# Performance work log

Measured on AMD Instinct MI355X. Metric: run time of the kernel, lower is better.

## Reference

```python
import jax, jax.numpy as jnp
import numpy as np

B, LENC, LDEC, DIN, H = 256, 48, 10, 512, 512
LOOK = 10  # hard-coded look_back in the torch module
START = LDEC + LENC - LOOK  # initial label index


def setup_inputs() -> dict:
    key = jax.random.key(0)
    ks = jax.random.split(key, 28)
    s = 0.05
    n = lambda k, shape: jax.random.normal(k, shape, jnp.float32) * s
    return {
        "input_p_q": jax.random.normal(ks[0], (B, LENC, DIN), jnp.float32),
        "label_p": jax.random.normal(ks[1], (B, LENC + LDEC), jnp.float32),
        # LSTMCell_spatial_encoder (input DIN)
        "Wih_sp": n(ks[2], (4 * H, DIN)), "Whh_sp": n(ks[3], (4 * H, H)),
        "bih_sp": n(ks[4], (4 * H,)), "bhh_sp": n(ks[5], (4 * H,)),
        # LSTMcell_target_encoder (input 1+H)
        "Wih_tg": n(ks[6], (4 * H, 1 + H)), "Whh_tg": n(ks[7], (4 * H, H)),
        "bih_tg": n(ks[8], (4 * H,)), "bhh_tg": n(ks[9], (4 * H,)),
        # LSTM_mid (single layer, input H)
        "Wih_mid": n(ks[10], (4 * H, H)), "Whh_mid": n(ks[11], (4 * H, H)),
        "bih_mid": n(ks[12], (4 * H,)), "bhh_mid": n(ks[13], (4 * H,)),
        # spatial attention
        "Wi_w": n(ks[14], (H, DIN)), "Wi_b": n(ks[15], (H,)),
        "We_w": n(ks[16], (H, 2 * H)), "Wt_w": n(ks[17], (H, 2 * H)),
        "Vd_w": n(ks[18], (DIN, H)), "Vd_b": n(ks[19], (DIN,)),
        # temporal attention
        "Wx_w": n(ks[20], (H, H)), "Wx_b": n(ks[21], (H,)),
        "Wh_w": n(ks[22], (H, 2 * H)),
        "V_w": n(ks[23], (1, H)), "V_b": n(ks[24], (1,)),
        "reg_w": n(ks[25], (1, H)), "reg_b": n(ks[26], (1,)),
    }


def _lstm_cell(x, h, c, Wih, Whh, b):
    # torch LSTMCell: gates ordered (i, f, g, o)
    g = x @ Wih.T + h @ Whh.T + b
    i, f, gg, o = jnp.split(g, 4, axis=1)
    c2 = jax.nn.sigmoid(f) * c + jax.nn.sigmoid(i) * jnp.tanh(gg)
    return jax.nn.sigmoid(o) * jnp.tanh(c2), c2


def reference(input_p_q, label_p, Wih_sp, Whh_sp, bih_sp, bhh_sp,
              Wih_tg, Whh_tg, bih_tg, bhh_tg, Wih_mid, Whh_mid, bih_mid, bhh_mid,
              Wi_w, Wi_b, We_w, Wt_w, Vd_w, Vd_b, Wx_w, Wx_b, Wh_w, V_w, V_b,
              reg_w, reg_b):
    Bsz = input_p_q.shape[0]
    b_sp = bih_sp + bhh_sp
    b_tg = bih_tg + bhh_tg
    b_mid = bih_mid + bhh_mid
    # Precompute spatial_attention_Wi(inputs) for all encoder steps: [LENC, B, H]
    wi_seq = jnp.transpose(jnp.einsum('bld,hd->blh', input_p_q, Wi_w) + Wi_b, (1, 0, 2))
    x_seq = jnp.transpose(input_p_q, (1, 0, 2))  # [LENC, B, DIN]
    zeros = jnp.zeros((Bsz, H), input_p_q.dtype)

    def outer_step(carry, _):
        ht, ct, dec_in, lab = carry
        x = jnp.concatenate([lab[:, None], dec_in], axis=1)          # [B, 1+H]
        ht, ct = _lstm_cell(x, ht, ct, Wih_tg, Whh_tg, b_tg)
        target = ht @ reg_w.T + reg_b                                # [B, 1]
        lab = target[:, 0]
        wt = jnp.concatenate([ht, ct], axis=1) @ Wt_w.T              # [B, H], fixed per inner loop

        def sp_step(c2, xs):
            he, ce = c2
            wi_x, x_i = xs
            score = jnp.tanh(jnp.concatenate([he, ce], axis=1) @ We_w.T + wi_x + wt) @ Vd_w.T + Vd_b
            x_mod = x_i * jax.nn.softmax(score, axis=1)              # [B, DIN]
            he, ce = _lstm_cell(x_mod, he, ce, Wih_sp, Whh_sp, b_sp)
            return (he, ce), he

        _, mid = jax.lax.scan(sp_step, (zeros, zeros), (wi_seq, x_seq))  # [LENC, B, H]

        def mid_step(c2, x_i):
            h, c = c2
            h, c = _lstm_cell(x_i, h, c, Wih_mid, Whh_mid, b_mid)
            return (h, c), h

        _, mid2 = jax.lax.scan(mid_step, (zeros, zeros), mid)        # [LENC, B, H]
        mid2 = jnp.transpose(mid2, (1, 0, 2))                        # [B, LENC, H]
        wh = jnp.concatenate([ht, ct], axis=1) @ Wh_w.T              # [B, H]
        sc = jnp.tanh(wh[:, None, :] + mid2 @ Wx_w.T + Wx_b) @ V_w.T + V_b  # [B, LENC, 1]
        # NOTE: torch uses the RAW (un-softmaxed) scores for the bmm
        dec_in = jnp.einsum('bl,blh->bh', sc[..., 0], mid2)          # [B, H]
        return (ht, ct, dec_in, lab), target[:, 0]

    init = (zeros, zeros, zeros, label_p[:, START])
    _, targets = jax.lax.scan(outer_step, init, None, length=LOOK)   # [LOOK, B]
    return targets.T                                                 # [B, LDEC]
```

## Files before the change

### kernel.cpp

```cpp
#include <hip/hip_runtime.h>
#include <math.h>

#define Bsz   256
#define Hd    512
#define Din   512
#define Lenc  48
#define Look  10
#define G4    2048
#define LabStride 58
#define StartIdx  48

typedef unsigned short u16;
using bfrag = __attribute__((ext_vector_type(8))) short;
using f32x4 = __attribute__((ext_vector_type(4))) float;

#define MFMA16(a,b,c) __builtin_amdgcn_mfma_f32_16x16x32_bf16((a),(b),(c),0,0,0)

__device__ __forceinline__ u16 f2bf(float f){
  unsigned u = __float_as_uint(f);
  u += 0x7FFFu + ((u>>16)&1u);
  return (u16)(u>>16);
}
__device__ __forceinline__ float bf2f(u16 h){ return __uint_as_float(((unsigned)h)<<16); }
__device__ __forceinline__ float sigm(float x){ return 1.f/(1.f+__expf(-x)); }

template<int K>
__device__ __forceinline__ void mm32(const u16* __restrict__ A, int lda,
                                     const u16* __restrict__ W, int ldw,
                                     f32x4* acc, int lane){
  const int rr = lane & 15, ko = (lane>>4)<<3;
  const u16* a0 = A + (size_t)rr*lda + ko;
  const u16* a1 = a0 + 16*(size_t)lda;
  const u16* w0 = W + (size_t)rr*ldw + ko;
  const u16* w1 = w0 + 16*(size_t)ldw;
#pragma unroll
  for(int k=0;k<K;k+=32){
    bfrag av0 = *(const bfrag*)(a0+k);
    bfrag av1 = *(const bfrag*)(a1+k);
    bfrag wv0 = *(const bfrag*)(w0+k);
    bfrag wv1 = *(const bfrag*)(w1+k);
    acc[0] = MFMA16(av0,wv0,acc[0]);
    acc[1] = MFMA16(av0,wv1,acc[1]);
    acc[2] = MFMA16(av1,wv0,acc[2]);
    acc[3] = MFMA16(av1,wv1,acc[3]);
  }
}

__global__ void k_cvt(const float* __restrict__ s, u16* __restrict__ d, int n){
  for(int i=blockIdx.x*blockDim.x+threadIdx.x; i<n; i+=gridDim.x*blockDim.x) d[i]=f2bf(s[i]);
}

__global__ void k_cvt_tg(const float* __restrict__ s, u16* __restrict__ d, float* __restrict__ c0){
  int stride=gridDim.x*blockDim.x;
  for(int i=blockIdx.x*blockDim.x+threadIdx.x; i<G4*Hd; i+=stride){
    int n=i>>9, k=i&511;
    d[i]=f2bf(s[n*513+1+k]);
  }
  for(int n=blockIdx.x*blockDim.x+threadIdx.x; n<G4; n+=stride) c0[n]=s[n*513];
}

__global__ void k_init(const float* __restrict__ label, float* __restrict__ lab){
  int b=threadIdx.x;
  if(b<Bsz) lab[b]=label[b*LabStride+StartIdx];
}

__global__ __launch_bounds__(64) void k_wi(const u16* __restrict__ inpb, const u16* __restrict__ Wi,
                     const float* __restrict__ Wib, float* __restrict__ wi_seq){
  int lane=threadIdx.x;
  int r0=blockIdx.x*32, h0=blockIdx.y*32;
  f32x4 acc[4]={};
  mm32<Din>(inpb+(size_t)r0*Din, Din, Wi+(size_t)h0*Din, Din, acc, lane);
  int cr=(lane>>4)*4, cc=lane&15;
  for(int mi=0;mi<2;mi++)for(int ni=0;ni<2;ni++){
    int h=h0+ni*16+cc; float bias=Wib[h];
    f32x4 a=acc[mi*2+ni];
    for(int j=0;j<4;j++){
      int g=r0+mi*16+cr+j;
      int b=g/Lenc, l=g-b*Lenc;
      wi_seq[((size_t)l*Bsz+b)*Hd + h] = a[j]+bias;
    }
  }
}


__global__ __launch_bounds__(128) void k_spre(const u16* __restrict__ he, const u16* __restrict__ ce,
      const u16* __restrict__ We, const float* __restrict__ wi_l, const float* __restrict__ wt,
      u16* __restrict__ spre, int zhc){
  int lane=threadIdx.x&63, wid=threadIdx.x>>6;
  int b0=blockIdx.x*32, h0=blockIdx.y*32;
  f32x4 acc[4]={};
  if(!zhc){
    if(wid==0) mm32<Hd>(he+(size_t)b0*Hd, Hd, We+(size_t)h0*1024,     1024, acc, lane);
    else       mm32<Hd>(ce+(size_t)b0*Hd, Hd, We+(size_t)h0*1024+512, 1024, acc, lane);
  }
  __shared__ f32x4 red[4*64];
  if(wid==1){ for(int i=0;i<4;i++) red[i*64+lane]=acc[i]; }
  __syncthreads();
  if(wid!=0) return;
  for(int i=0;i<4;i++) acc[i]+=red[i*64+lane];
  int cr=(lane>>4)*4, cc=lane&15;
  for(int mi=0;mi<2;mi++)for(int ni=0;ni<2;ni++){
    int h=h0+ni*16+cc;
    f32x4 a=acc[mi*2+ni];
    for(int j=0;j<4;j++){
      int b=b0+mi*16+cr+j;
      size_t ix=(size_t)b*Hd+h;
      spre[ix]=f2bf(tanhf(a[j]+wi_l[ix]+wt[ix]));
    }
  }
}

__global__ __launch_bounds__(128) void k_dual(const u16* __restrict__ A1, const u16* __restrict__ A2,
      const u16* __restrict__ W, float* __restrict__ C){
  int lane=threadIdx.x&63, wid=threadIdx.x>>6;
  int b0=blockIdx.x*32, h0=blockIdx.y*32;
  f32x4 acc[4]={};
  if(wid==0) mm32<Hd>(A1+(size_t)b0*Hd, Hd, W+(size_t)h0*1024,     1024, acc, lane);
  else       mm32<Hd>(A2+(size_t)b0*Hd, Hd, W+(size_t)h0*1024+512, 1024, acc, lane);
  __shared__ f32x4 red[4*64];
  if(wid==1){ for(int i=0;i<4;i++) red[i*64+lane]=acc[i]; }
  __syncthreads();
  if(wid!=0) return;
  for(int i=0;i<4;i++) acc[i]+=red[i*64+lane];
  int cr=(lane>>4)*4, cc=lane&15;
  for(int mi=0;mi<2;mi++)for(int ni=0;ni<2;ni++){
    int h=h0+ni*16+cc;
    f32x4 a=acc[mi*2+ni];
    for(int j=0;j<4;j++){
      int b=b0+mi*16+cr+j;
      C[(size_t)b*Hd+h]=a[j];
    }
  }
}

__global__ __launch_bounds__(128) void k_sgemm(const u16* __restrict__ spre, const u16* __restrict__ Vd,
      const float* __restrict__ Vdb, float* __restrict__ score){
  int lane=threadIdx.x&63, wid=threadIdx.x>>6;
  int b0=blockIdx.x*32, h0=blockIdx.y*32;
  f32x4 acc[4]={};
  mm32<256>(spre+(size_t)b0*Hd + wid*256, Hd, Vd+(size_t)h0*Hd + wid*256, Hd, acc, lane);
  __shared__ f32x4 red[4*64];
  if(wid==1){ for(int i=0;i<4;i++) red[i*64+lane]=acc[i]; }
  __syncthreads();
  if(wid!=0) return;
  for(int i=0;i<4;i++) acc[i]+=red[i*64+lane];
  int cr=(lane>>4)*4, cc=lane&15;
  for(int mi=0;mi<2;mi++)for(int ni=0;ni<2;ni++){
    int h=h0+ni*16+cc; float bias=Vdb[h];
    f32x4 a=acc[mi*2+ni];
    for(int j=0;j<4;j++){
      int b=b0+mi*16+cr+j;
      score[(size_t)b*Hd+h]=a[j]+bias;
    }
  }
}

__global__ __launch_bounds__(256) void k_softmax(const float* __restrict__ score,
      const float* __restrict__ inp, int l, u16* __restrict__ xmod){
  int b=blockIdx.x, tid=threadIdx.x;
  float s0=score[(size_t)b*Din+tid], s1=score[(size_t)b*Din+256+tid];
  float m=fmaxf(s0,s1);
  for(int o=1;o<64;o<<=1) m=fmaxf(m,__shfl_xor(m,o));
  __shared__ float r1[4], r2[4];
  if((tid&63)==0) r1[tid>>6]=m;
  __syncthreads();
  m=fmaxf(fmaxf(r1[0],r1[1]),fmaxf(r1[2],r1[3]));
  float e0=__expf(s0-m), e1=__expf(s1-m);
  float ss=e0+e1;
  for(int o=1;o<64;o<<=1) ss+=__shfl_xor(ss,o);
  if((tid&63)==0) r2[tid>>6]=ss;
  __syncthreads();
  float inv=1.f/(r2[0]+r2[1]+r2[2]+r2[3]);
  const float* xr = inp + ((size_t)b*Lenc+l)*Din;
  xmod[(size_t)b*Din+tid]     = f2bf(xr[tid]*e0*inv);
  xmod[(size_t)b*Din+256+tid] = f2bf(xr[256+tid]*e1*inv);
}

__global__ __launch_bounds__(128) void k_cell(const u16* __restrict__ A1, const u16* __restrict__ A2,
     const u16* __restrict__ Wih, const u16* __restrict__ Whh,
     const float* __restrict__ bih, const float* __restrict__ bhh,
     float* __restrict__ cst, u16* __restrict__ cbf, u16* __restrict__ hout, int l0){
  int lane=threadIdx.x&63, wid=threadIdx.x>>6;
  int b0=blockIdx.x*32, h0=blockIdx.y*32;
  f32x4 acc[4][4]={};
  if(wid==0){
    for(int g=0;g<4;g++) mm32<Hd>(A1+(size_t)b0*Hd, Hd, Wih+((size_t)g*Hd+h0)*Hd, Hd, acc[g], lane);
  } else if(!l0){
    for(int g=0;g<4;g++) mm32<Hd>(A2+(size_t)b0*Hd, Hd, Whh+((size_t)g*Hd+h0)*Hd, Hd, acc[g], lane);
  }
  __shared__ f32x4 red[16*64];
  if(wid==1){ for(int i=0;i<16;i++) red[i*64+lane]=acc[i>>2][i&3]; }
  __syncthreads();
  if(wid!=0) return;
  for(int i=0;i<16;i++) acc[i>>2][i&3]+=red[i*64+lane];
  int cr=(lane>>4)*4, cc=lane&15;
  for(int mi=0;mi<2;mi++)for(int ni=0;ni<2;ni++){
    int h=h0+ni*16+cc; int tq=mi*2+ni;
    float bi =bih[h]+bhh[h];
    float bff=bih[Hd+h]+bhh[Hd+h];
    float bg =bih[2*Hd+h]+bhh[2*Hd+h];
    float bo =bih[3*Hd+h]+bhh[3*Hd+h];
    for(int j=0;j<4;j++){
      int b=b0+mi*16+cr+j;
      size_t ix=(size_t)b*Hd+h;
      float ii=sigm(acc[0][tq][j]+bi);
      float ff=sigm(acc[1][tq][j]+bff);
      float gg=tanhf(acc[2][tq][j]+bg);
      float oo=sigm(acc[3][tq][j]+bo);
      float cold=l0?0.f:cst[ix];
      float c2=ff*cold+ii*gg;
      float hv=oo*tanhf(c2);
      cst[ix]=c2;
      if(cbf) cbf[ix]=f2bf(c2);
      hout[ix]=f2bf(hv);
    }
  }
}

__global__ __launch_bounds__(128) void k_tg(const u16* __restrict__ dec, const u16* __restrict__ ht,
    const u16* __restrict__ Wih, const u16* __restrict__ Whh,
    const float* __restrict__ c0, const float* __restrict__ bih, const float* __restrict__ bhh,
    const float* __restrict__ lab, float* __restrict__ cst, u16* __restrict__ cbf,
    u16* __restrict__ hout, int t0){
  int lane=threadIdx.x&63, wid=threadIdx.x>>6;
  int b0=blockIdx.x*32, h0=blockIdx.y*32;
  f32x4 acc[4][4]={};
  if(!t0){
    if(wid==0){ for(int g=0;g<4;g++) mm32<Hd>(dec+(size_t)b0*Hd, Hd, Wih+((size_t)g*Hd+h0)*Hd, Hd, acc[g], lane); }
    else      { for(int g=0;g<4;g++) mm32<Hd>(ht +(size_t)b0*Hd, Hd, Whh+((size_t)g*Hd+h0)*Hd, Hd, acc[g], lane); }
  }
  __shared__ f32x4 red[16*64];
  if(wid==1){ for(int i=0;i<16;i++) red[i*64+lane]=acc[i>>2][i&3]; }
  __syncthreads();
  if(wid!=0) return;
  for(int i=0;i<16;i++) acc[i>>2][i&3]+=red[i*64+lane];
  int cr=(lane>>4)*4, cc=lane&15;
  for(int mi=0;mi<2;mi++)for(int ni=0;ni<2;ni++){
    int h=h0+ni*16+cc; int tq=mi*2+ni;
    float bi =bih[h]+bhh[h];
    float bff=bih[Hd+h]+bhh[Hd+h];
    float bg =bih[2*Hd+h]+bhh[2*Hd+h];
    float bo =bih[3*Hd+h]+bhh[3*Hd+h];
    float ci=c0[h], cf=c0[Hd+h], cg=c0[2*Hd+h], co=c0[3*Hd+h];
    for(int j=0;j<4;j++){
      int b=b0+mi*16+cr+j;
      size_t ix=(size_t)b*Hd+h;
      float lb=lab[b];
      float ii=sigm(acc[0][tq][j]+bi +lb*ci);
      float ff=sigm(acc[1][tq][j]+bff+lb*cf);
      float gg=tanhf(acc[2][tq][j]+bg +lb*cg);
      float oo=sigm(acc[3][tq][j]+bo +lb*co);
      float cold=t0?0.f:cst[ix];
      float c2=ff*cold+ii*gg;
      float hv=oo*tanhf(c2);
      cst[ix]=c2; cbf[ix]=f2bf(c2); hout[ix]=f2bf(hv);
    }
  }
}

__global__ __launch_bounds__(64) void k_target(const u16* __restrict__ ht, const float* __restrict__ regw,
     const float* __restrict__ regb, float* __restrict__ outp, float* __restrict__ lab, int t){
  int b=blockIdx.x, lane=threadIdx.x;
  bfrag v=*(const bfrag*)(ht+(size_t)b*Hd+lane*8);
  const float* w=regw+lane*8;
  float a=0;
  for(int j=0;j<8;j++) a+=bf2f((u16)v[j])*w[j];
  for(int o=1;o<64;o<<=1) a+=__shfl_xor(a,o);
  if(lane==0){ float val=a+regb[0]; outp[b*Look+t]=val; lab[b]=val; }
}

__global__ __launch_bounds__(128) void k_scgemm(const u16* __restrict__ mid2, const u16* __restrict__ Wx,
      const float* __restrict__ Wxb, const float* __restrict__ wh, u16* __restrict__ TT){
  int lane=threadIdx.x&63, wid=threadIdx.x>>6;
  int r0=blockIdx.x*32, h0=blockIdx.y*32;
  f32x4 acc[4]={};
  mm32<256>(mid2+(size_t)r0*Hd + wid*256, Hd, Wx+(size_t)h0*Hd + wid*256, Hd, acc, lane);
  __shared__ f32x4 red[4*64];
  if(wid==1){ for(int i=0;i<4;i++) red[i*64+lane]=acc[i]; }
  __syncthreads();
  if(wid!=0) return;
  for(int i=0;i<4;i++) acc[i]+=red[i*64+lane];
  int cr=(lane>>4)*4, cc=lane&15;
  for(int mi=0;mi<2;mi++)for(int ni=0;ni<2;ni++){
    int h=h0+ni*16+cc; float wb=Wxb[h];
    f32x4 a=acc[mi*2+ni];
    for(int j=0;j<4;j++){
      int row=r0+mi*16+cr+j;
      int b=row&255;
      TT[(size_t)row*Hd+h]=f2bf(tanhf(a[j]+wh[(size_t)b*Hd+h]+wb));
    }
  }
}

__global__ __launch_bounds__(64) void k_scred(const u16* __restrict__ TT, const float* __restrict__ Vw,
      const float* __restrict__ Vb, float* __restrict__ sc){
  int row=blockIdx.x, lane=threadIdx.x;
  bfrag v=*(const bfrag*)(TT+(size_t)row*Hd+lane*8);
  const float* w=Vw+lane*8;
  float a=0;
  for(int j=0;j<8;j++) a+=bf2f((u16)v[j])*w[j];
  for(int o=1;o<64;o<<=1) a+=__shfl_xor(a,o);
  if(lane==0){ int l=row>>8, b=row&255; sc[b*Lenc+l]=a+Vb[0]; }
}

__global__ __launch_bounds__(256) void k_dec(const float* __restrict__ sc, const u16* __restrict__ mid2,
      u16* __restrict__ dec){
  __shared__ float s[Lenc];
  int b=blockIdx.x, tid=threadIdx.x;
  if(tid<Lenc) s[tid]=sc[b*Lenc+tid];
  __syncthreads();
  for(int h=tid; h<Hd; h+=256){
    float a=0;
    for(int l=0;l<Lenc;l++) a+=s[l]*bf2f(mid2[((size_t)l*Bsz+b)*Hd+h]);
    dec[(size_t)b*Hd+h]=f2bf(a);
  }
}

extern "C" void kernel_launch(void* const* d_in, const int* in_sizes, int n_in,
                              void* d_out, int out_size, void* d_ws, size_t ws_size,
                              hipStream_t stream){
  const float* f_inp    =(const float*)d_in[0];
  const float* f_label  =(const float*)d_in[1];
  const float* f_Wih_sp =(const float*)d_in[2];
  const float* f_Whh_sp =(const float*)d_in[3];
  const float* f_bih_sp =(const float*)d_in[4];
  const float* f_bhh_sp =(const float*)d_in[5];
  const float* f_Wih_tg =(const float*)d_in[6];
  const float* f_Whh_tg =(const float*)d_in[7];
  const float* f_bih_tg =(const float*)d_in[8];
  const float* f_bhh_tg =(const float*)d_in[9];
  const float* f_Wih_mid=(const float*)d_in[10];
  const float* f_Whh_mid=(const float*)d_in[11];
  const float* f_bih_mid=(const float*)d_in[12];
  const float* f_bhh_mid=(const float*)d_in[13];
  const float* f_Wi_w   =(const float*)d_in[14];
  const float* f_Wi_b   =(const float*)d_in[15];
  const float* f_We_w   =(const float*)d_in[16];
  const float* f_Wt_w   =(const float*)d_in[17];
  const float* f_Vd_w   =(const float*)d_in[18];
  const float* f_Vd_b   =(const float*)d_in[19];
  const float* f_Wx_w   =(const float*)d_in[20];
  const float* f_Wx_b   =(const float*)d_in[21];
  const float* f_Wh_w   =(const float*)d_in[22];
  const float* f_V_w    =(const float*)d_in[23];
  const float* f_V_b    =(const float*)d_in[24];
  const float* f_reg_w  =(const float*)d_in[25];
  const float* f_reg_b  =(const float*)d_in[26];
  float* outp=(float*)d_out;

  char* basep=(char*)d_ws; size_t off=0;
  auto alloc=[&](size_t bytes)->void*{ void* r=basep+off; off+=(bytes+255)&~((size_t)255); return r; };

  const size_t BH=(size_t)Bsz*Hd;
  u16*  wspih =(u16*)alloc((size_t)G4*Hd*2);
  u16*  wsphh =(u16*)alloc((size_t)G4*Hd*2);
  u16*  wtgih =(u16*)alloc((size_t)G4*Hd*2);
  u16*  wtghh =(u16*)alloc((size_t)G4*Hd*2);
  u16*  wmidih=(u16*)alloc((size_t)G4*Hd*2);
  u16*  wmidhh=(u16*)alloc((size_t)G4*Hd*2);
  u16*  web   =(u16*)alloc((size_t)Hd*1024*2);
  u16*  wtb   =(u16*)alloc((size_t)Hd*1024*2);
  u16*  whb   =(u16*)alloc((size_t)Hd*1024*2);
  u16*  vdb   =(u16*)alloc((size_t)Hd*Hd*2);
  u16*  wxb   =(u16*)alloc((size_t)Hd*Hd*2);
  u16*  wib   =(u16*)alloc((size_t)Hd*Hd*2);
  u16*  inpb  =(u16*)alloc((size_t)Bsz*Lenc*Din*2);
  float* c0f  =(float*)alloc((size_t)G4*4);
  float* wiseq=(float*)alloc((size_t)Lenc*BH*4);
  u16*  midb  =(u16*)alloc((size_t)Lenc*BH*2);
  u16*  mid2b =(u16*)alloc((size_t)Lenc*BH*2);
  u16*  ttb   =(u16*)alloc((size_t)Lenc*BH*2);
  u16*  spreb =(u16*)alloc(BH*2);
  float* scoref=(float*)alloc(BH*4);
  u16*  xmodb =(u16*)alloc(BH*2);
  float* cef  =(float*)alloc(BH*4);
  u16*  ceb   =(u16*)alloc(BH*2);
  float* ctf  =(float*)alloc(BH*4);
  u16*  ctb   =(u16*)alloc(BH*2);
  float* cmidf=(float*)alloc(BH*4);
  u16*  ht0   =(u16*)alloc(BH*2);
  u16*  ht1   =(u16*)alloc(BH*2);
  u16*  decb  =(u16*)alloc(BH*2);
  float* wtf  =(float*)alloc(BH*4);
  float* whf  =(float*)alloc(BH*4);
  float* labf =(float*)alloc((size_t)Bsz*4);
  float* scf  =(float*)alloc((size_t)Bsz*Lenc*4);

  dim3 cvtg(512), cvtb(256);
  k_cvt<<<cvtg,cvtb,0,stream>>>(f_Wih_sp ,wspih ,G4*Hd);
  k_cvt<<<cvtg,cvtb,0,stream>>>(f_Whh_sp ,wsphh ,G4*Hd);
  k_cvt<<<cvtg,cvtb,0,stream>>>(f_Whh_tg ,wtghh ,G4*Hd);
  k_cvt<<<cvtg,cvtb,0,stream>>>(f_Wih_mid,wmidih,G4*Hd);
  k_cvt<<<cvtg,cvtb,0,stream>>>(f_Whh_mid,wmidhh,G4*Hd);
  k_cvt<<<cvtg,cvtb,0,stream>>>(f_We_w   ,web   ,Hd*1024);
  k_cvt<<<cvtg,cvtb,0,stream>>>(f_Wt_w   ,wtb   ,Hd*1024);
  k_cvt<<<cvtg,cvtb,0,stream>>>(f_Wh_w   ,whb   ,Hd*1024);
  k_cvt<<<cvtg,cvtb,0,stream>>>(f_Vd_w   ,vdb   ,Hd*Hd);
  k_cvt<<<cvtg,cvtb,0,stream>>>(f_Wx_w   ,wxb   ,Hd*Hd);
  k_cvt<<<cvtg,cvtb,0,stream>>>(f_Wi_w   ,wib   ,Hd*Hd);
  k_cvt<<<dim3(1024),cvtb,0,stream>>>(f_inp, inpb, Bsz*Lenc*Din);
  k_cvt_tg<<<cvtg,cvtb,0,stream>>>(f_Wih_tg, wtgih, c0f);
  k_init<<<dim3(1),dim3(256),0,stream>>>(f_label, labf);
  k_wi<<<dim3(384,16),dim3(64),0,stream>>>(inpb, wib, f_Wi_b, wiseq);

  dim3 g816(8,16), b128(128);
  u16 *htR=ht0, *htW=ht1;
  for(int t=0;t<Look;t++){
    int t0 = (t==0)?1:0;
    k_tg<<<g816,b128,0,stream>>>(decb, htR, wtgih, wtghh, c0f, f_bih_tg, f_bhh_tg,
                                 labf, ctf, ctb, htW, t0);
    k_target<<<dim3(Bsz),dim3(64),0,stream>>>(htW, f_reg_w, f_reg_b, outp, labf, t);
    k_dual<<<g816,b128,0,stream>>>(htW, ctb, wtb, wtf);
    k_dual<<<g816,b128,0,stream>>>(htW, ctb, whb, whf);

    for(int l=0;l<Lenc;l++){
      int l0=(l==0)?1:0;
      const u16* hprev = l0 ? midb : (midb + (size_t)(l-1)*BH);
      k_spre<<<g816,b128,0,stream>>>(hprev, ceb, web, wiseq+(size_t)l*BH, wtf, spreb, l0);
      k_sgemm<<<g816,b128,0,stream>>>(spreb, vdb, f_Vd_b, scoref);
      k_softmax<<<dim3(Bsz),dim3(256),0,stream>>>(scoref, f_inp, l, xmodb);
      k_cell<<<g816,b128,0,stream>>>(xmodb, hprev, wspih, wsphh, f_bih_sp, f_bhh_sp,
                                     cef, ceb, midb+(size_t)l*BH, l0);
    }
    for(int l=0;l<Lenc;l++){
      int l0=(l==0)?1:0;
      const u16* hprev = l0 ? mid2b : (mid2b + (size_t)(l-1)*BH);
      k_cell<<<g816,b128,0,stream>>>(midb+(size_t)l*BH, hprev, wmidih, wmidhh,
                                     f_bih_mid, f_bhh_mid, cmidf, (u16*)nullptr,
                                     mid2b+(size_t)l*BH, l0);
    }
    k_scgemm<<<dim3(384,16),b128,0,stream>>>(mid2b, wxb, f_Wx_b, whf, ttb);
    k_scred<<<dim3(Lenc*Bsz),dim3(64),0,stream>>>(ttb, f_V_w, f_V_b, scf);
    k_dec<<<dim3(Bsz),dim3(256),0,stream>>>(scf, mid2b, decb);

    u16* tmp=htR; htR=htW; htW=tmp;
  }
}
```

Before: 35.63 ms.

## Fuse softmax into spatial cell, pipeline mid-LSTM with spatial loop, merge dual GEMMs

The softmax over attention scores now runs inside the spatial LSTM cell kernel, which writes the modulated input into shared memory and uses it directly as the GEMM operand. The mid-layer LSTM step l-1 is computed in extra z-blocks of the spre kernel during spatial step l, which removes the separate 48-step serial mid loop and adds parallelism to small launches. The two k_dual launches are merged into one launch with a z-dimension. Together these cut kernel launch count and serial depth per outer step, at the cost of redundant softmax work, since each of the 16 h-blocks recomputes it for its 32 batch rows.

```diff
diff --git a/kernel.cpp b/kernel.cpp
--- a/kernel.cpp
+++ b/kernel.cpp
@@ -82,36 +82,11 @@
   }
 }
 
-
-__global__ __launch_bounds__(128) void k_spre(const u16* __restrict__ he, const u16* __restrict__ ce,
-      const u16* __restrict__ We, const float* __restrict__ wi_l, const float* __restrict__ wt,
-      u16* __restrict__ spre, int zhc){
-  int lane=threadIdx.x&63, wid=threadIdx.x>>6;
-  int b0=blockIdx.x*32, h0=blockIdx.y*32;
-  f32x4 acc[4]={};
-  if(!zhc){
-    if(wid==0) mm32<Hd>(he+(size_t)b0*Hd, Hd, We+(size_t)h0*1024,     1024, acc, lane);
-    else       mm32<Hd>(ce+(size_t)b0*Hd, Hd, We+(size_t)h0*1024+512, 1024, acc, lane);
-  }
-  __shared__ f32x4 red[4*64];
-  if(wid==1){ for(int i=0;i<4;i++) red[i*64+lane]=acc[i]; }
-  __syncthreads();
-  if(wid!=0) return;
-  for(int i=0;i<4;i++) acc[i]+=red[i*64+lane];
-  int cr=(lane>>4)*4, cc=lane&15;
-  for(int mi=0;mi<2;mi++)for(int ni=0;ni<2;ni++){
-    int h=h0+ni*16+cc;
-    f32x4 a=acc[mi*2+ni];
-    for(int j=0;j<4;j++){
-      int b=b0+mi*16+cr+j;
-      size_t ix=(size_t)b*Hd+h;
-      spre[ix]=f2bf(tanhf(a[j]+wi_l[ix]+wt[ix]));
-    }
-  }
-}
-
-__global__ __launch_bounds__(128) void k_dual(const u16* __restrict__ A1, const u16* __restrict__ A2,
-      const u16* __restrict__ W, float* __restrict__ C){
+__global__ __launch_bounds__(128) void k_dual2(const u16* __restrict__ A1, const u16* __restrict__ A2,
+      const u16* __restrict__ W0, const u16* __restrict__ W1,
+      float* __restrict__ C0, float* __restrict__ C1){
+  const u16* W = blockIdx.z ? W1 : W0;
+  float*     C = blockIdx.z ? C1 : C0;
   int lane=threadIdx.x&63, wid=threadIdx.x>>6;
   int b0=blockIdx.x*32, h0=blockIdx.y*32;
   f32x4 acc[4]={};
@@ -129,6 +104,71 @@
     for(int j=0;j<4;j++){
       int b=b0+mi*16+cr+j;
       C[(size_t)b*Hd+h]=a[j];
+    }
+  }
+}
+
+__global__ __launch_bounds__(128) void k_spre_mid(
+      const u16* __restrict__ he, const u16* __restrict__ ce, const u16* __restrict__ web,
+      const float* __restrict__ wi_l, const float* __restrict__ wt, u16* __restrict__ spre, int zhc,
+      const u16* __restrict__ mx, const u16* __restrict__ mh,
+      const u16* __restrict__ wmih, const u16* __restrict__ wmhh,
+      const float* __restrict__ bihm, const float* __restrict__ bhhm,
+      float* __restrict__ cmid, u16* __restrict__ mout, int men, int ml0){
+  __shared__ f32x4 red[16*64];
+  int lane=threadIdx.x&63, wid=threadIdx.x>>6;
+  int b0=blockIdx.x*32, h0=blockIdx.y*32;
+  int cr=(lane>>4)*4, cc=lane&15;
+
+  if(blockIdx.z==0){
+    f32x4 acc[4]={};
+    if(!zhc){
+      if(wid==0) mm32<Hd>(he+(size_t)b0*Hd, Hd, web+(size_t)h0*1024,     1024, acc, lane);
+      else       mm32<Hd>(ce+(size_t)b0*Hd, Hd, web+(size_t)h0*1024+512, 1024, acc, lane);
+    }
+    if(wid==1){ for(int i=0;i<4;i++) red[i*64+lane]=acc[i]; }
+    __syncthreads();
+    if(wid!=0) return;
+    for(int i=0;i<4;i++) acc[i]+=red[i*64+lane];
+    for(int mi=0;mi<2;mi++)for(int ni=0;ni<2;ni++){
+      int h=h0+ni*16+cc;
+      f32x4 a=acc[mi*2+ni];
+      for(int j=0;j<4;j++){
+        int b=b0+mi*16+cr+j;
+        size_t ix=(size_t)b*Hd+h;
+        spre[ix]=f2bf(tanhf(a[j]+wi_l[ix]+wt[ix]));
+      }
+    }
+  } else {
+    if(!men) return;
+    f32x4 acc[4][4]={};
+    if(wid==0){
+      for(int g=0;g<4;g++) mm32<Hd>(mx+(size_t)b0*Hd, Hd, wmih+((size_t)g*Hd+h0)*Hd, Hd, acc[g], lane);
+    } else if(!ml0){
+      for(int g=0;g<4;g++) mm32<Hd>(mh+(size_t)b0*Hd, Hd, wmhh+((size_t)g*Hd+h0)*Hd, Hd, acc[g], lane);
+    }
+    if(wid==1){ for(int i=0;i<16;i++) red[i*64+lane]=acc[i>>2][i&3]; }
+    __syncthreads();
+    if(wid!=0) return;
+    for(int i=0;i<16;i++) acc[i>>2][i&3]+=red[i*64+lane];
+    for(int mi=0;mi<2;mi++)for(int ni=0;ni<2;ni++){
+      int h=h0+ni*16+cc; int tq=mi*2+ni;
+      float bi =bihm[h]+bhhm[h];
+      float bff=bihm[Hd+h]+bhhm[Hd+h];
+      float bg =bihm[2*Hd+h]+bhhm[2*Hd+h];
+      float bo =bihm[3*Hd+h]+bhhm[3*Hd+h];
+      for(int j=0;j<4;j++){
+        int b=b0+mi*16+cr+j;
+        size_t ix=(size_t)b*Hd+h;
+        float ii=sigm(acc[0][tq][j]+bi);
+        float ff=sigm(acc[1][tq][j]+bff);
+        float gg=tanhf(acc[2][tq][j]+bg);
+        float oo=sigm(acc[3][tq][j]+bo);
+        float cold=ml0?0.f:cmid[ix];
+        float c2=ff*cold+ii*gg;
+        cmid[ix]=c2;
+        mout[ix]=f2bf(oo*tanhf(c2));
+      }
     }
   }
 }
@@ -155,25 +195,83 @@
   }
 }
 
-__global__ __launch_bounds__(256) void k_softmax(const float* __restrict__ score,
-      const float* __restrict__ inp, int l, u16* __restrict__ xmod){
-  int b=blockIdx.x, tid=threadIdx.x;
-  float s0=score[(size_t)b*Din+tid], s1=score[(size_t)b*Din+256+tid];
-  float m=fmaxf(s0,s1);
-  for(int o=1;o<64;o<<=1) m=fmaxf(m,__shfl_xor(m,o));
-  __shared__ float r1[4], r2[4];
-  if((tid&63)==0) r1[tid>>6]=m;
-  __syncthreads();
-  m=fmaxf(fmaxf(r1[0],r1[1]),fmaxf(r1[2],r1[3]));
-  float e0=__expf(s0-m), e1=__expf(s1-m);
-  float ss=e0+e1;
-  for(int o=1;o<64;o<<=1) ss+=__shfl_xor(ss,o);
-  if((tid&63)==0) r2[tid>>6]=ss;
-  __syncthreads();
-  float inv=1.f/(r2[0]+r2[1]+r2[2]+r2[3]);
-  const float* xr = inp + ((size_t)b*Lenc+l)*Din;
-  xmod[(size_t)b*Din+tid]     = f2bf(xr[tid]*e0*inv);
-  xmod[(size_t)b*Din+256+tid] = f2bf(xr[256+tid]*e1*inv);
+#define XP 520
+__global__ __launch_bounds__(128) void k_cellF(const float* __restrict__ score,
+     const float* __restrict__ finp, int l,
+     const u16* __restrict__ hprev, const u16* __restrict__ Wih, const u16* __restrict__ Whh,
+     const float* __restrict__ bih, const float* __restrict__ bhh,
+     float* __restrict__ cst, u16* __restrict__ cbf, u16* __restrict__ hout, int l0){
+  __shared__ __align__(16) u16 xm[32*XP];
+  __shared__ f32x4 red[16*64];
+  int tid=threadIdx.x, lane=tid&63, wid=tid>>6;
+  int b0=blockIdx.x*32, h0=blockIdx.y*32;
+
+  {
+    int r=tid>>2, q=tid&3;
+    int b=b0+r;
+    const float* srow = score + (size_t)b*Hd + q*128;
+    const float* xrow = finp + ((size_t)b*Lenc + l)*Din + q*128;
+    float m=-1e30f;
+    for(int j=0;j<128;j+=4){
+      float4 v=*(const float4*)(srow+j);
+      m=fmaxf(m,fmaxf(fmaxf(v.x,v.y),fmaxf(v.z,v.w)));
+    }
+    m=fmaxf(m,__shfl_xor(m,1));
+    m=fmaxf(m,__shfl_xor(m,2));
+    float ssum=0.f;
+    for(int j=0;j<128;j+=4){
+      float4 v=*(const float4*)(srow+j);
+      ssum+=__expf(v.x-m)+__expf(v.y-m)+__expf(v.z-m)+__expf(v.w-m);
+    }
+    ssum+=__shfl_xor(ssum,1);
+    ssum+=__shfl_xor(ssum,2);
+    float inv=1.f/ssum;
+    for(int j=0;j<128;j+=4){
+      float4 v=*(const float4*)(srow+j);
+      float4 x=*(const float4*)(xrow+j);
+      ushort4 o;
+      o.x=f2bf(x.x*__expf(v.x-m)*inv);
+      o.y=f2bf(x.y*__expf(v.y-m)*inv);
+      o.z=f2bf(x.z*__expf(v.z-m)*inv);
+      o.w=f2bf(x.w*__expf(v.w-m)*inv);
+      *(ushort4*)(&xm[r*XP + q*128 + j]) = o;
+    }
+  }
+  __syncthreads();
+
+  f32x4 acc[4][4]={};
+  if(wid==0){
+    for(int g=0;g<4;g++) mm32<Hd>((const u16*)xm, XP, Wih+((size_t)g*Hd+h0)*Hd, Hd, acc[g], lane);
+  } else if(!l0){
+    for(int g=0;g<4;g++) mm32<Hd>(hprev+(size_t)b0*Hd, Hd, Whh+((size_t)g*Hd+h0)*Hd, Hd, acc[g], lane);
+  }
+  __syncthreads();
+  if(wid==1){ for(int i=0;i<16;i++) red[i*64+lane]=acc[i>>2][i&3]; }
+  __syncthreads();
+  if(wid!=0) return;
+  for(int i=0;i<16;i++) acc[i>>2][i&3]+=red[i*64+lane];
+  int cr=(lane>>4)*4, cc=lane&15;
+  for(int mi=0;mi<2;mi++)for(int ni=0;ni<2;ni++){
+    int h=h0+ni*16+cc; int tq=mi*2+ni;
+    float bi =bih[h]+bhh[h];
+    float bff=bih[Hd+h]+bhh[Hd+h];
+    float bg =bih[2*Hd+h]+bhh[2*Hd+h];
+    float bo =bih[3*Hd+h]+bhh[3*Hd+h];
+    for(int j=0;j<4;j++){
+      int b=b0+mi*16+cr+j;
+      size_t ix=(size_t)b*Hd+h;
+      float ii=sigm(acc[0][tq][j]+bi);
+      float ff=sigm(acc[1][tq][j]+bff);
+      float gg=tanhf(acc[2][tq][j]+bg);
+      float oo=sigm(acc[3][tq][j]+bo);
+      float cold=l0?0.f:cst[ix];
+      float c2=ff*cold+ii*gg;
+      float hv=oo*tanhf(c2);
+      cst[ix]=c2;
+      cbf[ix]=f2bf(c2);
+      hout[ix]=f2bf(hv);
+    }
+  }
 }
 
 __global__ __launch_bounds__(128) void k_cell(const u16* __restrict__ A1, const u16* __restrict__ A2,
@@ -241,14 +339,14 @@
     float bff=bih[Hd+h]+bhh[Hd+h];
     float bg =bih[2*Hd+h]+bhh[2*Hd+h];
     float bo =bih[3*Hd+h]+bhh[3*Hd+h];
-    float ci=c0[h], cf=c0[Hd+h], cg=c0[2*Hd+h], co=c0[3*Hd+h];
+    float ci=c0[h], cf=c0[Hd+h], cg2=c0[2*Hd+h], co=c0[3*Hd+h];
     for(int j=0;j<4;j++){
       int b=b0+mi*16+cr+j;
       size_t ix=(size_t)b*Hd+h;
       float lb=lab[b];
       float ii=sigm(acc[0][tq][j]+bi +lb*ci);
       float ff=sigm(acc[1][tq][j]+bff+lb*cf);
-      float gg=tanhf(acc[2][tq][j]+bg +lb*cg);
+      float gg=tanhf(acc[2][tq][j]+bg +lb*cg2);
       float oo=sigm(acc[3][tq][j]+bo +lb*co);
       float cold=t0?0.f:cst[ix];
       float c2=ff*cold+ii*gg;
@@ -372,7 +470,6 @@
   u16*  ttb   =(u16*)alloc((size_t)Lenc*BH*2);
   u16*  spreb =(u16*)alloc(BH*2);
   float* scoref=(float*)alloc(BH*4);
-  u16*  xmodb =(u16*)alloc(BH*2);
   float* cef  =(float*)alloc(BH*4);
   u16*  ceb   =(u16*)alloc(BH*2);
   float* ctf  =(float*)alloc(BH*4);
@@ -403,32 +500,32 @@
   k_init<<<dim3(1),dim3(256),0,stream>>>(f_label, labf);
   k_wi<<<dim3(384,16),dim3(64),0,stream>>>(inpb, wib, f_Wi_b, wiseq);
 
-  dim3 g816(8,16), b128(128);
+  dim3 g816(8,16), g816z2(8,16,2), b128(128);
   u16 *htR=ht0, *htW=ht1;
   for(int t=0;t<Look;t++){
     int t0 = (t==0)?1:0;
     k_tg<<<g816,b128,0,stream>>>(decb, htR, wtgih, wtghh, c0f, f_bih_tg, f_bhh_tg,
                                  labf, ctf, ctb, htW, t0);
     k_target<<<dim3(Bsz),dim3(64),0,stream>>>(htW, f_reg_w, f_reg_b, outp, labf, t);
-    k_dual<<<g816,b128,0,stream>>>(htW, ctb, wtb, wtf);
-    k_dual<<<g816,b128,0,stream>>>(htW, ctb, whb, whf);
+    k_dual2<<<g816z2,b128,0,stream>>>(htW, ctb, wtb, whb, wtf, whf);
 
     for(int l=0;l<Lenc;l++){
       int l0=(l==0)?1:0;
       const u16* hprev = l0 ? midb : (midb + (size_t)(l-1)*BH);
-      k_spre<<<g816,b128,0,stream>>>(hprev, ceb, web, wiseq+(size_t)l*BH, wtf, spreb, l0);
+      const u16* mx = l0 ? midb  : (midb  + (size_t)(l-1)*BH);
+      const u16* mh = (l<=1) ? mid2b : (mid2b + (size_t)(l-2)*BH);
+      u16* mout = l0 ? mid2b : (mid2b + (size_t)(l-1)*BH);
+      k_spre_mid<<<g816z2,b128,0,stream>>>(hprev, ceb, web, wiseq+(size_t)l*BH, wtf, spreb, l0,
+                                           mx, mh, wmidih, wmidhh, f_bih_mid, f_bhh_mid,
+                                           cmidf, mout, (l>=1)?1:0, (l==1)?1:0);
       k_sgemm<<<g816,b128,0,stream>>>(spreb, vdb, f_Vd_b, scoref);
-      k_softmax<<<dim3(Bsz),dim3(256),0,stream>>>(scoref, f_inp, l, xmodb);
-      k_cell<<<g816,b128,0,stream>>>(xmodb, hprev, wspih, wsphh, f_bih_sp, f_bhh_sp,
-                                     cef, ceb, midb+(size_t)l*BH, l0);
-    }
-    for(int l=0;l<Lenc;l++){
-      int l0=(l==0)?1:0;
-      const u16* hprev = l0 ? mid2b : (mid2b + (size_t)(l-1)*BH);
-      k_cell<<<g816,b128,0,stream>>>(midb+(size_t)l*BH, hprev, wmidih, wmidhh,
-                                     f_bih_mid, f_bhh_mid, cmidf, (u16*)nullptr,
-                                     mid2b+(size_t)l*BH, l0);
-    }
+      k_cellF<<<g816,b128,0,stream>>>(scoref, f_inp, l, hprev, wspih, wsphh,
+                                      f_bih_sp, f_bhh_sp, cef, ceb, midb+(size_t)l*BH, l0);
+    }
+    k_cell<<<g816,b128,0,stream>>>(midb+(size_t)47*BH, mid2b+(size_t)46*BH, wmidih, wmidhh,
+                                   f_bih_mid, f_bhh_mid, cmidf, (u16*)nullptr,
+                                   mid2b+(size_t)47*BH, 0);
+
     k_scgemm<<<dim3(384,16),b128,0,stream>>>(mid2b, wxb, f_Wx_b, whf, ttb);
     k_scred<<<dim3(Lenc*Bsz),dim3(64),0,stream>>>(ttb, f_V_w, f_V_b, scf);
     k_dec<<<dim3(Bsz),dim3(256),0,stream>>>(scf, mid2b, decb);
```

New measurement: 31.46 ms. -11.7%, faster.
